# Kernel tuning notes

Hardware: AMD Instinct MI355X
Metric: run time of the kernel (lower is better)

## Reference

```python
import jax, jax.numpy as jnp
import numpy as np

B, S, D = 8, 1024, 768
H, HD = 12, 64  # heads, head dim (H*HD == D)
EPS = 1e-12


def setup_inputs() -> dict:
    key = jax.random.key(0)
    ks = jax.random.split(key, 8)
    s = 0.02
    return {
        "hidden_states": jax.random.normal(ks[0], (B, S, D), jnp.float32),
        "attention_mask": jnp.zeros((B, 1, 1, S), jnp.float32),
        "head_mask": jnp.ones((H,), jnp.float32),
        "Wq": jax.random.normal(ks[1], (D, H * HD), jnp.float32) * s,
        "bq": jnp.zeros((H * HD,), jnp.float32),
        "Wk": jax.random.normal(ks[2], (D, H * HD), jnp.float32) * s,
        "bk": jnp.zeros((H * HD,), jnp.float32),
        "Wv": jax.random.normal(ks[3], (D, H * HD), jnp.float32) * s,
        "bv": jnp.zeros((H * HD,), jnp.float32),
        "Wo": jax.random.normal(ks[4], (D, H * HD), jnp.float32) * s,  # torch Linear weight [out=D, in=H*HD]
        "bo": jnp.zeros((D,), jnp.float32),
        "gamma": jnp.ones((D,), jnp.float32),
        "beta": jnp.zeros((D,), jnp.float32),
    }


def reference(hidden_states, attention_mask, head_mask, Wq, bq, Wk, bk, Wv, bv, Wo, bo, gamma, beta):
    def heads(x):  # [B,S,H*HD] -> [B,H,S,HD]
        return x.reshape(B, S, H, HD).transpose(0, 2, 1, 3)

    q = heads(hidden_states @ Wq.T + bq)
    k = heads(hidden_states @ Wk.T + bk)
    v = heads(hidden_states @ Wv.T + bv)

    scores = jnp.einsum("bhqd,bhkd->bhqk", q, k) / np.sqrt(HD).astype(np.float32)
    scores = scores + attention_mask
    probs = jax.nn.softmax(scores, axis=-1)  # dropout p=0 (eval)
    ctx = jnp.einsum("bhqk,bhkd->bhqd", probs, v)  # [B,H,S,HD]

    # masked per-head output projection: Wo.T.view(H, HD, D)
    Wph = Wo.T.reshape(H, HD, D)
    proj = jnp.einsum("bhsd,hde,h->bse", ctx, Wph, head_mask) + bo

    # residual + LayerNorm
    x = proj + hidden_states
    mu = jnp.mean(x, axis=-1, keepdims=True)
    var = jnp.mean(jnp.square(x - mu), axis=-1, keepdims=True)
    out = (x - mu) * jax.lax.rsqrt(var + EPS) * gamma + beta
    return out
```

## Files before the change

kernel.cpp:

```cpp
#include <hip/hip_runtime.h>
#include <hip/hip_bf16.h>
#include <math.h>

#define Bn 8
#define Sn 1024
#define Dn 768
#define Hn 12
#define MROWS (Bn * Sn)

typedef __attribute__((ext_vector_type(8))) short short8;
typedef __attribute__((ext_vector_type(4))) float floatx4;

__device__ __forceinline__ unsigned short f2b(float x) {
    union { float f; unsigned u; } v; v.f = x;
    unsigned r = v.u + 0x7fffu + ((v.u >> 16) & 1u);
    return (unsigned short)(r >> 16);
}

__device__ __forceinline__ unsigned pk2(float a, float b) {
    union { __hip_bfloat162 h; unsigned u; } v;
    v.h = __float22bfloat162_rn(float2{a, b});
    return v.u;
}

__device__ __forceinline__ float fexp2(float x) {
    float r;
    asm("v_exp_f32 %0, %1" : "=v"(r) : "v"(x));
    return r;
}

__device__ __forceinline__ void gload16(const void* g, void* l) {
    __builtin_amdgcn_global_load_lds(
        (const __attribute__((address_space(1))) void*)g,
        (__attribute__((address_space(3))) void*)l, 16, 0, 0);
}

#define MEMFENCE() asm volatile("" ::: "memory")
#define WAITV8()  asm volatile("s_waitcnt vmcnt(8)" ::: "memory")
#define WAITV6()  asm volatile("s_waitcnt vmcnt(6)" ::: "memory")
#define WAITV0()  asm volatile("s_waitcnt vmcnt(0)" ::: "memory")
#define WAITLGKM() asm volatile("s_waitcnt lgkmcnt(0)" ::: "memory")

__global__ __launch_bounds__(256) void convert_all(const float* __restrict__ X,
                                                   const float* __restrict__ Wq, const float* __restrict__ Wk,
                                                   const float* __restrict__ Wv, const float* __restrict__ Wo,
                                                   unsigned short* __restrict__ Xb,
                                                   unsigned short* __restrict__ Wqb, unsigned short* __restrict__ Wkb,
                                                   unsigned short* __restrict__ Wvb, unsigned short* __restrict__ Wob) {
    const int id = blockIdx.x;
    const float* src;
    unsigned short* dst;
    int i;
    if (id < 6144) {
        src = X; dst = Xb;
        i = id * 256 + threadIdx.x;
    } else {
        const int y = (id - 6144) / 576;
        src = (y == 0) ? Wq : (y == 1) ? Wk : (y == 2) ? Wv : Wo;
        dst = (y == 0) ? Wqb : (y == 1) ? Wkb : (y == 2) ? Wvb : Wob;
        i = ((id - 6144) % 576) * 256 + threadIdx.x;
    }
    float4 v = reinterpret_cast<const float4*>(src)[i];
    ushort4 o;
    o.x = f2b(v.x); o.y = f2b(v.y); o.z = f2b(v.z); o.w = f2b(v.w);
    reinterpret_cast<ushort4*>(dst)[i] = o;
}

#define QKV_COMPUTE(Ab, Wb)                                                    \
    {                                                                          \
        short8 af[4][2], bf[4][2];                                             \
        _Pragma("unroll") for (int i = 0; i < 4; i++)                          \
            _Pragma("unroll") for (int ks = 0; ks < 2; ks++) {                 \
                af[i][ks] = *(const short8*)&(Ab)[aoff[i][ks]];                \
                bf[i][ks] = *(const short8*)&(Wb)[woff[i][ks]];                \
            }                                                                  \
        __builtin_amdgcn_s_setprio(1);                                         \
        _Pragma("unroll") for (int ks = 0; ks < 2; ks++)                       \
            _Pragma("unroll") for (int i = 0; i < 4; i++)                      \
                _Pragma("unroll") for (int j = 0; j < 4; j++)                  \
                    acc[i][j] = __builtin_amdgcn_mfma_f32_16x16x32_bf16(       \
                        af[i][ks], bf[j][ks], acc[i][j], 0, 0, 0);             \
        __builtin_amdgcn_s_setprio(0);                                         \
    }

__global__ __launch_bounds__(256) void gemm_qkv(const unsigned short* __restrict__ A,
                                                const unsigned short* __restrict__ Wq,
                                                const unsigned short* __restrict__ Wk,
                                                const unsigned short* __restrict__ Wv,
                                                const float* __restrict__ bq,
                                                const float* __restrict__ bk,
                                                const float* __restrict__ bv,
                                                unsigned short* __restrict__ Qh,
                                                unsigned short* __restrict__ Kh,
                                                unsigned short* __restrict__ Vt) {
    __shared__ __align__(16) unsigned short As[2][128 * 64];
    __shared__ __align__(16) unsigned short Ws[2][128 * 64];
    const int orig = blockIdx.x;
    const int chunk = orig & 7;
    const int local = orig >> 3;
    const int by = chunk * 8 + local / 18;
    const int bxr = local % 18;
    const int mat = bxr / 6;
    const int m0 = by * 128;
    const int n0 = (bxr % 6) * 128;
    const unsigned short* W = (mat == 0) ? Wq : (mat == 1) ? Wk : Wv;
    const float* bias = (mat == 0) ? bq : (mat == 1) ? bk : bv;
    unsigned short* Cout = (mat == 0) ? Qh : (mat == 1) ? Kh : Vt;

    const int tid = threadIdx.x;
    const int w = tid >> 6, l = tid & 63, quad = l >> 4, mr = l & 15;
    const int wm = (w >> 1) * 64, wn = (w & 1) * 64;

    const unsigned short* gAsrc[4];
    const unsigned short* gWsrc[4];
    unsigned short* lAdst[4];
    unsigned short* lWdst[4];
#pragma unroll
    for (int j = 0; j < 4; j++) {
        const int u = tid + j * 256;
        const int r = u >> 3, c = u & 7;
        const int kq = (c ^ (r & 7)) * 8;
        gAsrc[j] = &A[(size_t)(m0 + r) * Dn + kq];
        gWsrc[j] = &W[(size_t)(n0 + r) * Dn + kq];
        lAdst[j] = &As[0][u * 8];
        lWdst[j] = &Ws[0][u * 8];
    }

    int aoff[4][2], woff[4][2];
#pragma unroll
    for (int i = 0; i < 4; i++) {
        const int ra = wm + i * 16 + mr;
        const int rw = wn + i * 16 + mr;
#pragma unroll
        for (int ks = 0; ks < 2; ks++) {
            aoff[i][ks] = (ra * 8 + ((quad + ks * 4) ^ (ra & 7))) * 8;
            woff[i][ks] = (rw * 8 + ((quad + ks * 4) ^ (rw & 7))) * 8;
        }
    }

    floatx4 acc[4][4];
#pragma unroll
    for (int i = 0; i < 4; i++)
#pragma unroll
        for (int j = 0; j < 4; j++) {
            floatx4 z = {0.f, 0.f, 0.f, 0.f};
            acc[i][j] = z;
        }

    const unsigned short* Af = &As[0][0];
    const unsigned short* Wf = &Ws[0][0];

#pragma unroll
    for (int j = 0; j < 4; j++) {
        gload16(gAsrc[j], lAdst[j]);
        gload16(gWsrc[j], lWdst[j]);
    }

    for (int kt = 0; kt < 12; kt += 2) {
        {
            const int k0 = (kt + 1) * 64;
#pragma unroll
            for (int j = 0; j < 4; j++) {
                gload16(gAsrc[j] + k0, lAdst[j] + 8192);
                gload16(gWsrc[j] + k0, lWdst[j] + 8192);
            }
        }
        WAITV8();
        __builtin_amdgcn_s_barrier();
        MEMFENCE();
        QKV_COMPUTE(Af, Wf);
        __builtin_amdgcn_s_barrier();
        MEMFENCE();

        if (kt + 2 < 12) {
            const int k0 = (kt + 2) * 64;
#pragma unroll
            for (int j = 0; j < 4; j++) {
                gload16(gAsrc[j] + k0, lAdst[j]);
                gload16(gWsrc[j] + k0, lWdst[j]);
            }
            WAITV8();
        } else {
            WAITV0();
        }
        __builtin_amdgcn_s_barrier();
        MEMFENCE();
        QKV_COMPUTE(Af + 8192, Wf + 8192);
        __builtin_amdgcn_s_barrier();
        MEMFENCE();
    }

#pragma unroll
    for (int j = 0; j < 4; j++) {
        const int col = n0 + wn + j * 16 + mr;
        const float bval = bias[col];
        const int h = col >> 6, d = col & 63;
#pragma unroll
        for (int i = 0; i < 4; i++) {
            const int mbase = m0 + wm + i * 16 + quad * 4;
            const int b = mbase >> 10, s0 = mbase & 1023;
            const size_t base = (size_t)(b * Hn + h) << 16;
            if (mat == 2) {
                ushort4 o;
                o.x = f2b(acc[i][j][0] + bval);
                o.y = f2b(acc[i][j][1] + bval);
                o.z = f2b(acc[i][j][2] + bval);
                o.w = f2b(acc[i][j][3] + bval);
                *reinterpret_cast<ushort4*>(&Cout[base + (size_t)d * 1024 + s0]) = o;
            } else {
#pragma unroll
                for (int r = 0; r < 4; r++) {
                    const float val = acc[i][j][r] + bval;
                    Cout[base + (size_t)(s0 + r) * 64 + d] = f2b(val);
                }
            }
        }
    }
}

#define OUT_COMPUTE(Ab, Wb)                                                    \
    {                                                                          \
        short8 af[4][2], bf[2][2];                                             \
        _Pragma("unroll") for (int i = 0; i < 4; i++)                          \
            _Pragma("unroll") for (int ks = 0; ks < 2; ks++)                   \
                af[i][ks] = *(const short8*)&(Ab)[aoff[i][ks]];                \
        _Pragma("unroll") for (int j = 0; j < 2; j++)                          \
            _Pragma("unroll") for (int ks = 0; ks < 2; ks++)                   \
                bf[j][ks] = *(const short8*)&(Wb)[woff[j][ks]];                \
        __builtin_amdgcn_s_setprio(1);                                         \
        _Pragma("unroll") for (int ks = 0; ks < 2; ks++)                       \
            _Pragma("unroll") for (int i = 0; i < 4; i++)                      \
                _Pragma("unroll") for (int j = 0; j < 2; j++)                  \
                    acc[i][j] = __builtin_amdgcn_mfma_f32_16x16x32_bf16(       \
                        af[i][ks], bf[j][ks], acc[i][j], 0, 0, 0);             \
        __builtin_amdgcn_s_setprio(0);                                         \
    }

__global__ __launch_bounds__(256) void gemm_out(const unsigned short* __restrict__ A,
                                                const unsigned short* __restrict__ W,
                                                const float* __restrict__ bias,
                                                const float* __restrict__ X,
                                                float* __restrict__ xres) {
    __shared__ __align__(16) unsigned short As[2][64 * 64];
    __shared__ __align__(16) unsigned short Ws[2][128 * 64];
    const int orig = blockIdx.x;
    const int chunk = orig & 7;
    const int local = orig >> 3;
    const int by = chunk * 16 + local / 6;
    const int bx = local % 6;
    const int m0 = by * 64;
    const int n0 = bx * 128;

    const int tid = threadIdx.x;
    const int w = tid >> 6, l = tid & 63, quad = l >> 4, mr = l & 15;

    const unsigned short* gAsrc[2];
    unsigned short* lAdst[2];
#pragma unroll
    for (int j = 0; j < 2; j++) {
        const int u = tid + j * 256;
        const int r = u >> 3, c = u & 7;
        gAsrc[j] = &A[(size_t)(m0 + r) * Dn + (c ^ (r & 7)) * 8];
        lAdst[j] = &As[0][u * 8];
    }
    const unsigned short* gWsrc[4];
    unsigned short* lWdst[4];
#pragma unroll
    for (int j = 0; j < 4; j++) {
        const int u = tid + j * 256;
        const int r = u >> 3, c = u & 7;
        gWsrc[j] = &W[(size_t)(n0 + r) * Dn + (c ^ (r & 7)) * 8];
        lWdst[j] = &Ws[0][u * 8];
    }

    int aoff[4][2], woff[2][2];
#pragma unroll
    for (int i = 0; i < 4; i++) {
        const int ra = i * 16 + mr;
#pragma unroll
        for (int ks = 0; ks < 2; ks++)
            aoff[i][ks] = (ra * 8 + ((quad + ks * 4) ^ (ra & 7))) * 8;
    }
#pragma unroll
    for (int j = 0; j < 2; j++) {
        const int rw = w * 32 + j * 16 + mr;
#pragma unroll
        for (int ks = 0; ks < 2; ks++)
            woff[j][ks] = (rw * 8 + ((quad + ks * 4) ^ (rw & 7))) * 8;
    }

    floatx4 acc[4][2];
#pragma unroll
    for (int i = 0; i < 4; i++)
#pragma unroll
        for (int j = 0; j < 2; j++) {
            floatx4 z = {0.f, 0.f, 0.f, 0.f};
            acc[i][j] = z;
        }

    const unsigned short* Af = &As[0][0];
    const unsigned short* Wf = &Ws[0][0];

#pragma unroll
    for (int j = 0; j < 2; j++) gload16(gAsrc[j], lAdst[j]);
#pragma unroll
    for (int j = 0; j < 4; j++) gload16(gWsrc[j], lWdst[j]);

    for (int kt = 0; kt < 12; kt += 2) {
        {
            const int k0 = (kt + 1) * 64;
#pragma unroll
            for (int j = 0; j < 2; j++) gload16(gAsrc[j] + k0, lAdst[j] + 4096);
#pragma unroll
            for (int j = 0; j < 4; j++) gload16(gWsrc[j] + k0, lWdst[j] + 8192);
        }
        WAITV6();
        __builtin_amdgcn_s_barrier();
        MEMFENCE();
        OUT_COMPUTE(Af, Wf);
        __builtin_amdgcn_s_barrier();
        MEMFENCE();

        if (kt + 2 < 12) {
            const int k0 = (kt + 2) * 64;
#pragma unroll
            for (int j = 0; j < 2; j++) gload16(gAsrc[j] + k0, lAdst[j]);
#pragma unroll
            for (int j = 0; j < 4; j++) gload16(gWsrc[j] + k0, lWdst[j]);
            WAITV6();
        } else {
            WAITV0();
        }
        __builtin_amdgcn_s_barrier();
        MEMFENCE();
        OUT_COMPUTE(Af + 4096, Wf + 8192);
        __builtin_amdgcn_s_barrier();
        MEMFENCE();
    }

#pragma unroll
    for (int j = 0; j < 2; j++) {
        const int col = n0 + w * 32 + j * 16 + mr;
        const float bval = bias[col];
#pragma unroll
        for (int i = 0; i < 4; i++) {
#pragma unroll
            for (int r = 0; r < 4; r++) {
                const int m = m0 + i * 16 + quad * 4 + r;
                xres[(size_t)m * Dn + col] = acc[i][j][r] + bval + X[(size_t)m * Dn + col];
            }
        }
    }
}

__global__ __launch_bounds__(256) void flash_attn_mfma(const unsigned short* __restrict__ Qh,
                                                       const unsigned short* __restrict__ Kh,
                                                       const unsigned short* __restrict__ Vt,
                                                       const float* __restrict__ mask,
                                                       const float* __restrict__ head_mask,
                                                       unsigned short* __restrict__ ctx) {
    __shared__ __align__(16) unsigned short Ks[64 * 72];
    __shared__ __align__(16) unsigned short Vs[64 * 72];
    __shared__ __align__(16) unsigned short Ps[128 * 72];
    __shared__ float msk[64];

    const float LOG2E = 1.44269504088896f;
    const float C1 = 0.125f * 1.44269504088896f;

    const int orig = blockIdx.x;
    const int chunk = orig & 7;
    const int local = orig >> 3;
    const int bh = chunk * 12 + local / 8;
    const int qt = local % 8;
    const int b = bh / Hn, h = bh % Hn;
    const int q0 = qt * 128;
    const int tid = threadIdx.x;
    const int w = tid >> 6, l = tid & 63, quad = l >> 4, mr = l & 15;
    const size_t hb = (size_t)(b * Hn + h) << 16;

    short8 aq[2][2];
#pragma unroll
    for (int j = 0; j < 2; j++)
#pragma unroll
        for (int ks = 0; ks < 2; ks++)
            aq[j][ks] = *(const short8*)&Qh[hb + (size_t)(q0 + w * 32 + j * 16 + mr) * 64 + ks * 32 + quad * 8];

    float l_s[2] = {0.f, 0.f};
    floatx4 oacc[2][4];
#pragma unroll
    for (int i = 0; i < 2; i++)
#pragma unroll
        for (int jj = 0; jj < 4; jj++) {
            floatx4 z = {0.f, 0.f, 0.f, 0.f};
            oacc[i][jj] = z;
        }

    const int srow = tid >> 2;
    const int scol = (tid & 3) * 16;

    short8 pk0 = *(const short8*)&Kh[hb + (size_t)srow * 64 + scol];
    short8 pk1 = *(const short8*)&Kh[hb + (size_t)srow * 64 + scol + 8];
    short8 pv0 = *(const short8*)&Vt[hb + (size_t)srow * 1024 + scol];
    short8 pv1 = *(const short8*)&Vt[hb + (size_t)srow * 1024 + scol + 8];
    float pm = mask[b * Sn + (tid & 63)];

    for (int kt = 0; kt < Sn / 64; kt++) {
        __builtin_amdgcn_s_barrier();
        MEMFENCE();
        *(short8*)&Ks[srow * 72 + scol] = pk0;
        *(short8*)&Ks[srow * 72 + scol + 8] = pk1;
        *(short8*)&Vs[srow * 72 + scol] = pv0;
        *(short8*)&Vs[srow * 72 + scol + 8] = pv1;
        if (tid < 64) msk[tid] = pm * LOG2E;
        if (kt < Sn / 64 - 1) {
            const int k0 = (kt + 1) * 64;
            pk0 = *(const short8*)&Kh[hb + (size_t)(k0 + srow) * 64 + scol];
            pk1 = *(const short8*)&Kh[hb + (size_t)(k0 + srow) * 64 + scol + 8];
            pv0 = *(const short8*)&Vt[hb + (size_t)srow * 1024 + k0 + scol];
            pv1 = *(const short8*)&Vt[hb + (size_t)srow * 1024 + k0 + scol + 8];
            pm = mask[b * Sn + k0 + (tid & 63)];
        }
        WAITLGKM();
        __builtin_amdgcn_s_barrier();
        MEMFENCE();

        floatx4 sacc[4][2];
#pragma unroll
        for (int i = 0; i < 4; i++)
#pragma unroll
            for (int j = 0; j < 2; j++) {
                floatx4 z = {0.f, 0.f, 0.f, 0.f};
                sacc[i][j] = z;
            }
#pragma unroll
        for (int ks = 0; ks < 2; ks++) {
            short8 kfr[4];
#pragma unroll
            for (int i = 0; i < 4; i++)
                kfr[i] = *(const short8*)&Ks[(i * 16 + mr) * 72 + ks * 32 + quad * 8];
            __builtin_amdgcn_s_setprio(1);
#pragma unroll
            for (int i = 0; i < 4; i++)
#pragma unroll
                for (int j = 0; j < 2; j++)
                    sacc[i][j] = __builtin_amdgcn_mfma_f32_16x16x32_bf16(kfr[i], aq[j][ks], sacc[i][j], 0, 0, 0);
            __builtin_amdgcn_s_setprio(0);
        }

#pragma unroll
        for (int i = 0; i < 4; i++) {
            floatx4 mk4 = *(const floatx4*)&msk[i * 16 + quad * 4];
#pragma unroll
            for (int j = 0; j < 2; j++) {
                float p[4];
#pragma unroll
                for (int r = 0; r < 4; r++) {
                    p[r] = fexp2(sacc[i][j][r] * C1 + mk4[r]);
                    l_s[j] += p[r];
                }
                uint2 w2;
                w2.x = pk2(p[0], p[1]);
                w2.y = pk2(p[2], p[3]);
                *(uint2*)&Ps[(w * 32 + j * 16 + mr) * 72 + i * 16 + quad * 4] = w2;
            }
        }

#pragma unroll
        for (int ks = 0; ks < 2; ks++) {
            short8 ap0 = *(const short8*)&Ps[(w * 32 + mr) * 72 + ks * 32 + quad * 8];
            short8 ap1 = *(const short8*)&Ps[(w * 32 + 16 + mr) * 72 + ks * 32 + quad * 8];
            __builtin_amdgcn_s_setprio(1);
#pragma unroll
            for (int jj = 0; jj < 4; jj++) {
                short8 bv = *(const short8*)&Vs[(jj * 16 + mr) * 72 + ks * 32 + quad * 8];
                oacc[0][jj] = __builtin_amdgcn_mfma_f32_16x16x32_bf16(ap0, bv, oacc[0][jj], 0, 0, 0);
                oacc[1][jj] = __builtin_amdgcn_mfma_f32_16x16x32_bf16(ap1, bv, oacc[1][jj], 0, 0, 0);
            }
            __builtin_amdgcn_s_setprio(0);
        }
    }

    float L[2];
#pragma unroll
    for (int j = 0; j < 2; j++) {
        float t = l_s[j];
        t += __shfl_xor(t, 16);
        t += __shfl_xor(t, 32);
        L[j] = t;
    }
    const float hm = head_mask[h];
    float inv[2][4];
#pragma unroll
    for (int i = 0; i < 2; i++)
#pragma unroll
        for (int r = 0; r < 4; r++)
            inv[i][r] = hm / __shfl(L[i], quad * 4 + r);

#pragma unroll
    for (int i = 0; i < 2; i++)
#pragma unroll
        for (int jj = 0; jj < 4; jj++)
#pragma unroll
            for (int r = 0; r < 4; r++) {
                const int qrow = q0 + w * 32 + i * 16 + quad * 4 + r;
                ctx[(size_t)(b * Sn + qrow) * Dn + h * 64 + jj * 16 + mr] = f2b(oacc[i][jj][r] * inv[i][r]);
            }
}

__global__ __launch_bounds__(256) void ln_kernel(const float* __restrict__ x,
                                                 const float* __restrict__ gamma,
                                                 const float* __restrict__ beta,
                                                 float* __restrict__ out) {
    __shared__ float r1[4];
    __shared__ float r2[4];
    const int m = blockIdx.x;
    const int tid = threadIdx.x;
    const int w = tid >> 6, lane = tid & 63;

    float xv[3];
    float s = 0.f, ss = 0.f;
#pragma unroll
    for (int i = 0; i < 3; i++) {
        int j = tid + i * 256;
        float t = x[(size_t)m * Dn + j];
        xv[i] = t;
        s += t;
        ss += t * t;
    }
#pragma unroll
    for (int o = 1; o < 64; o <<= 1) {
        s += __shfl_xor(s, o);
        ss += __shfl_xor(ss, o);
    }
    if (lane == 0) { r1[w] = s; r2[w] = ss; }
    __syncthreads();
    const float sum = r1[0] + r1[1] + r1[2] + r1[3];
    const float sqs = r2[0] + r2[1] + r2[2] + r2[3];
    const float mu = sum * (1.0f / Dn);
    const float var = sqs * (1.0f / Dn) - mu * mu;
    const float rstd = rsqrtf(var + 1e-12f);
#pragma unroll
    for (int i = 0; i < 3; i++) {
        int j = tid + i * 256;
        out[(size_t)m * Dn + j] = (xv[i] - mu) * rstd * gamma[j] + beta[j];
    }
}

extern "C" void kernel_launch(void* const* d_in, const int* in_sizes, int n_in,
                              void* d_out, int out_size, void* d_ws, size_t ws_size,
                              hipStream_t stream) {
    const float* X         = (const float*)d_in[0];
    const float* mask      = (const float*)d_in[1];
    const float* head_mask = (const float*)d_in[2];
    const float* Wq        = (const float*)d_in[3];
    const float* bq        = (const float*)d_in[4];
    const float* Wk        = (const float*)d_in[5];
    const float* bk        = (const float*)d_in[6];
    const float* Wv        = (const float*)d_in[7];
    const float* bv        = (const float*)d_in[8];
    const float* Wo        = (const float*)d_in[9];
    const float* bo        = (const float*)d_in[10];
    const float* gamma     = (const float*)d_in[11];
    const float* beta      = (const float*)d_in[12];
    float* out = (float*)d_out;

    const size_t NE = (size_t)Bn * Sn * Dn;
    const size_t NW = (size_t)Dn * Dn;

    char* p = (char*)d_ws;
    unsigned short* Xb  = (unsigned short*)p;  p += NE * 2;
    unsigned short* Wqb = (unsigned short*)p;  p += NW * 2;
    unsigned short* Wkb = (unsigned short*)p;  p += NW * 2;
    unsigned short* Wvb = (unsigned short*)p;  p += NW * 2;
    unsigned short* Wob = (unsigned short*)p;  p += NW * 2;
    unsigned short* Qh  = (unsigned short*)p;  p += NE * 2;
    unsigned short* Kh  = (unsigned short*)p;  p += NE * 2;
    unsigned short* Vtb = (unsigned short*)p;  p += NE * 2;
    unsigned short* ctx = (unsigned short*)p;  p += NE * 2;
    float* xres = (float*)p;

    convert_all<<<8448, 256, 0, stream>>>(X, Wq, Wk, Wv, Wo, Xb, Wqb, Wkb, Wvb, Wob);

    gemm_qkv<<<1152, 256, 0, stream>>>(Xb, Wqb, Wkb, Wvb, bq, bk, bv, Qh, Kh, Vtb);

    flash_attn_mfma<<<768, 256, 0, stream>>>(Qh, Kh, Vtb, mask, head_mask, ctx);

    gemm_out<<<768, 256, 0, stream>>>(ctx, Wob, bo, X, xres);

    ln_kernel<<<MROWS, 256, 0, stream>>>(xres, gamma, beta, out);
}
```

Measured before the change: 215.3 us.

## Enlarge GEMM tiles to 256x256 and 128x256 with 512-thread blocks

Both projection GEMMs now use 512-thread blocks with larger output tiles. The QKV GEMM goes from 128x128 to 256x256 with 8x4 MFMA tiles per wave, and the output GEMM goes from 64x128 to 128x256 with 4x4 tiles per wave. The inner MFMA loop is reordered to load one B fragment at a time, which eases register pressure. The aim is more data reuse per LDS load and fewer global loads per FLOP. The cost is far fewer blocks (288 and 192 on a device with about 256 CUs), which risks poor occupancy and wave-quantization imbalance, plus much higher LDS and register use.

```diff
diff --git a/kernel.cpp b/kernel.cpp
--- a/kernel.cpp
+++ b/kernel.cpp
@@ -68,48 +68,49 @@
 
 #define QKV_COMPUTE(Ab, Wb)                                                    \
     {                                                                          \
-        short8 af[4][2], bf[4][2];                                             \
-        _Pragma("unroll") for (int i = 0; i < 4; i++)                          \
-            _Pragma("unroll") for (int ks = 0; ks < 2; ks++) {                 \
-                af[i][ks] = *(const short8*)&(Ab)[aoff[i][ks]];                \
-                bf[i][ks] = *(const short8*)&(Wb)[woff[i][ks]];                \
+        _Pragma("unroll") for (int ks = 0; ks < 2; ks++) {                     \
+            short8 af[8];                                                      \
+            _Pragma("unroll") for (int i = 0; i < 8; i++)                      \
+                af[i] = *(const short8*)&(Ab)[aoff[i][ks]];                    \
+            __builtin_amdgcn_s_setprio(1);                                     \
+            _Pragma("unroll") for (int j = 0; j < 4; j++) {                    \
+                short8 bf = *(const short8*)&(Wb)[woff[j][ks]];                \
+                _Pragma("unroll") for (int i = 0; i < 8; i++)                  \
+                    acc[i][j] = __builtin_amdgcn_mfma_f32_16x16x32_bf16(       \
+                        af[i], bf, acc[i][j], 0, 0, 0);                        \
             }                                                                  \
-        __builtin_amdgcn_s_setprio(1);                                         \
-        _Pragma("unroll") for (int ks = 0; ks < 2; ks++)                       \
-            _Pragma("unroll") for (int i = 0; i < 4; i++)                      \
-                _Pragma("unroll") for (int j = 0; j < 4; j++)                  \
-                    acc[i][j] = __builtin_amdgcn_mfma_f32_16x16x32_bf16(       \
-                        af[i][ks], bf[j][ks], acc[i][j], 0, 0, 0);             \
-        __builtin_amdgcn_s_setprio(0);                                         \
-    }
-
-__global__ __launch_bounds__(256) void gemm_qkv(const unsigned short* __restrict__ A,
-                                                const unsigned short* __restrict__ Wq,
-                                                const unsigned short* __restrict__ Wk,
-                                                const unsigned short* __restrict__ Wv,
-                                                const float* __restrict__ bq,
-                                                const float* __restrict__ bk,
-                                                const float* __restrict__ bv,
-                                                unsigned short* __restrict__ Qh,
-                                                unsigned short* __restrict__ Kh,
-                                                unsigned short* __restrict__ Vt) {
-    __shared__ __align__(16) unsigned short As[2][128 * 64];
-    __shared__ __align__(16) unsigned short Ws[2][128 * 64];
+            __builtin_amdgcn_s_setprio(0);                                     \
+        }                                                                      \
+    }
+
+__global__ __launch_bounds__(512, 2) void gemm_qkv(const unsigned short* __restrict__ A,
+                                                   const unsigned short* __restrict__ Wq,
+                                                   const unsigned short* __restrict__ Wk,
+                                                   const unsigned short* __restrict__ Wv,
+                                                   const float* __restrict__ bq,
+                                                   const float* __restrict__ bk,
+                                                   const float* __restrict__ bv,
+                                                   unsigned short* __restrict__ Qh,
+                                                   unsigned short* __restrict__ Kh,
+                                                   unsigned short* __restrict__ Vt) {
+    __shared__ __align__(16) unsigned short As[2][256 * 64];
+    __shared__ __align__(16) unsigned short Ws[2][256 * 64];
     const int orig = blockIdx.x;
     const int chunk = orig & 7;
     const int local = orig >> 3;
-    const int by = chunk * 8 + local / 18;
-    const int bxr = local % 18;
-    const int mat = bxr / 6;
-    const int m0 = by * 128;
-    const int n0 = (bxr % 6) * 128;
+    const int by = chunk * 4 + local / 9;
+    const int bxr = local % 9;
+    const int mat = bxr / 3;
+    const int m0 = by * 256;
+    const int n0 = (bxr % 3) * 256;
     const unsigned short* W = (mat == 0) ? Wq : (mat == 1) ? Wk : Wv;
     const float* bias = (mat == 0) ? bq : (mat == 1) ? bk : bv;
     unsigned short* Cout = (mat == 0) ? Qh : (mat == 1) ? Kh : Vt;
 
     const int tid = threadIdx.x;
     const int w = tid >> 6, l = tid & 63, quad = l >> 4, mr = l & 15;
-    const int wm = (w >> 1) * 64, wn = (w & 1) * 64;
+    const int wm = (w >> 2) * 128;
+    const int wn = (w & 3) * 64;
 
     const unsigned short* gAsrc[4];
     const unsigned short* gWsrc[4];
@@ -117,7 +118,7 @@
     unsigned short* lWdst[4];
 #pragma unroll
     for (int j = 0; j < 4; j++) {
-        const int u = tid + j * 256;
+        const int u = tid + j * 512;
         const int r = u >> 3, c = u & 7;
         const int kq = (c ^ (r & 7)) * 8;
         gAsrc[j] = &A[(size_t)(m0 + r) * Dn + kq];
@@ -126,21 +127,25 @@
         lWdst[j] = &Ws[0][u * 8];
     }
 
-    int aoff[4][2], woff[4][2];
-#pragma unroll
-    for (int i = 0; i < 4; i++) {
+    int aoff[8][2], woff[4][2];
+#pragma unroll
+    for (int i = 0; i < 8; i++) {
         const int ra = wm + i * 16 + mr;
-        const int rw = wn + i * 16 + mr;
-#pragma unroll
-        for (int ks = 0; ks < 2; ks++) {
+#pragma unroll
+        for (int ks = 0; ks < 2; ks++)
             aoff[i][ks] = (ra * 8 + ((quad + ks * 4) ^ (ra & 7))) * 8;
-            woff[i][ks] = (rw * 8 + ((quad + ks * 4) ^ (rw & 7))) * 8;
-        }
-    }
-
-    floatx4 acc[4][4];
-#pragma unroll
-    for (int i = 0; i < 4; i++)
+    }
+#pragma unroll
+    for (int j = 0; j < 4; j++) {
+        const int rw = wn + j * 16 + mr;
+#pragma unroll
+        for (int ks = 0; ks < 2; ks++)
+            woff[j][ks] = (rw * 8 + ((quad + ks * 4) ^ (rw & 7))) * 8;
+    }
+
+    floatx4 acc[8][4];
+#pragma unroll
+    for (int i = 0; i < 8; i++)
 #pragma unroll
         for (int j = 0; j < 4; j++) {
             floatx4 z = {0.f, 0.f, 0.f, 0.f};
@@ -161,8 +166,8 @@
             const int k0 = (kt + 1) * 64;
 #pragma unroll
             for (int j = 0; j < 4; j++) {
-                gload16(gAsrc[j] + k0, lAdst[j] + 8192);
-                gload16(gWsrc[j] + k0, lWdst[j] + 8192);
+                gload16(gAsrc[j] + k0, lAdst[j] + 16384);
+                gload16(gWsrc[j] + k0, lWdst[j] + 16384);
             }
         }
         WAITV8();
@@ -185,7 +190,7 @@
         }
         __builtin_amdgcn_s_barrier();
         MEMFENCE();
-        QKV_COMPUTE(Af + 8192, Wf + 8192);
+        QKV_COMPUTE(Af + 16384, Wf + 16384);
         __builtin_amdgcn_s_barrier();
         MEMFENCE();
     }
@@ -196,7 +201,7 @@
         const float bval = bias[col];
         const int h = col >> 6, d = col & 63;
 #pragma unroll
-        for (int i = 0; i < 4; i++) {
+        for (int i = 0; i < 8; i++) {
             const int mbase = m0 + wm + i * 16 + quad * 4;
             const int b = mbase >> 10, s0 = mbase & 1023;
             const size_t base = (size_t)(b * Hn + h) << 16;
@@ -220,45 +225,46 @@
 
 #define OUT_COMPUTE(Ab, Wb)                                                    \
     {                                                                          \
-        short8 af[4][2], bf[2][2];                                             \
-        _Pragma("unroll") for (int i = 0; i < 4; i++)                          \
-            _Pragma("unroll") for (int ks = 0; ks < 2; ks++)                   \
-                af[i][ks] = *(const short8*)&(Ab)[aoff[i][ks]];                \
-        _Pragma("unroll") for (int j = 0; j < 2; j++)                          \
-            _Pragma("unroll") for (int ks = 0; ks < 2; ks++)                   \
-                bf[j][ks] = *(const short8*)&(Wb)[woff[j][ks]];                \
-        __builtin_amdgcn_s_setprio(1);                                         \
-        _Pragma("unroll") for (int ks = 0; ks < 2; ks++)                       \
+        _Pragma("unroll") for (int ks = 0; ks < 2; ks++) {                     \
+            short8 af[4];                                                      \
             _Pragma("unroll") for (int i = 0; i < 4; i++)                      \
-                _Pragma("unroll") for (int j = 0; j < 2; j++)                  \
+                af[i] = *(const short8*)&(Ab)[aoff[i][ks]];                    \
+            __builtin_amdgcn_s_setprio(1);                                     \
+            _Pragma("unroll") for (int j = 0; j < 4; j++) {                    \
+                short8 bf = *(const short8*)&(Wb)[woff[j][ks]];                \
+                _Pragma("unroll") for (int i = 0; i < 4; i++)                  \
                     acc[i][j] = __builtin_amdgcn_mfma_f32_16x16x32_bf16(       \
-                        af[i][ks], bf[j][ks], acc[i][j], 0, 0, 0);             \
-        __builtin_amdgcn_s_setprio(0);                                         \
-    }
-
-__global__ __launch_bounds__(256) void gemm_out(const unsigned short* __restrict__ A,
-                                                const unsigned short* __restrict__ W,
-                                                const float* __restrict__ bias,
-                                                const float* __restrict__ X,
-                                                float* __restrict__ xres) {
-    __shared__ __align__(16) unsigned short As[2][64 * 64];
-    __shared__ __align__(16) unsigned short Ws[2][128 * 64];
+                        af[i], bf, acc[i][j], 0, 0, 0);                        \
+            }                                                                  \
+            __builtin_amdgcn_s_setprio(0);                                     \
+        }                                                                      \
+    }
+
+__global__ __launch_bounds__(512, 2) void gemm_out(const unsigned short* __restrict__ A,
+                                                   const unsigned short* __restrict__ W,
+                                                   const float* __restrict__ bias,
+                                                   const float* __restrict__ X,
+                                                   float* __restrict__ xres) {
+    __shared__ __align__(16) unsigned short As[2][128 * 64];
+    __shared__ __align__(16) unsigned short Ws[2][256 * 64];
     const int orig = blockIdx.x;
     const int chunk = orig & 7;
     const int local = orig >> 3;
-    const int by = chunk * 16 + local / 6;
-    const int bx = local % 6;
-    const int m0 = by * 64;
-    const int n0 = bx * 128;
+    const int by = chunk * 8 + local / 3;
+    const int bx = local % 3;
+    const int m0 = by * 128;
+    const int n0 = bx * 256;
 
     const int tid = threadIdx.x;
     const int w = tid >> 6, l = tid & 63, quad = l >> 4, mr = l & 15;
+    const int wm = (w >> 2) * 64;
+    const int wn = (w & 3) * 64;
 
     const unsigned short* gAsrc[2];
     unsigned short* lAdst[2];
 #pragma unroll
     for (int j = 0; j < 2; j++) {
-        const int u = tid + j * 256;
+        const int u = tid + j * 512;
         const int r = u >> 3, c = u & 7;
         gAsrc[j] = &A[(size_t)(m0 + r) * Dn + (c ^ (r & 7)) * 8];
         lAdst[j] = &As[0][u * 8];
@@ -267,33 +273,33 @@
     unsigned short* lWdst[4];
 #pragma unroll
     for (int j = 0; j < 4; j++) {
-        const int u = tid + j * 256;
+        const int u = tid + j * 512;
         const int r = u >> 3, c = u & 7;
         gWsrc[j] = &W[(size_t)(n0 + r) * Dn + (c ^ (r & 7)) * 8];
         lWdst[j] = &Ws[0][u * 8];
     }
 
-    int aoff[4][2], woff[2][2];
+    int aoff[4][2], woff[4][2];
 #pragma unroll
     for (int i = 0; i < 4; i++) {
-        const int ra = i * 16 + mr;
+        const int ra = wm + i * 16 + mr;
 #pragma unroll
         for (int ks = 0; ks < 2; ks++)
             aoff[i][ks] = (ra * 8 + ((quad + ks * 4) ^ (ra & 7))) * 8;
     }
 #pragma unroll
-    for (int j = 0; j < 2; j++) {
-        const int rw = w * 32 + j * 16 + mr;
+    for (int j = 0; j < 4; j++) {
+        const int rw = wn + j * 16 + mr;
 #pragma unroll
         for (int ks = 0; ks < 2; ks++)
             woff[j][ks] = (rw * 8 + ((quad + ks * 4) ^ (rw & 7))) * 8;
     }
 
-    floatx4 acc[4][2];
+    floatx4 acc[4][4];
 #pragma unroll
     for (int i = 0; i < 4; i++)
 #pragma unroll
-        for (int j = 0; j < 2; j++) {
+        for (int j = 0; j < 4; j++) {
             floatx4 z = {0.f, 0.f, 0.f, 0.f};
             acc[i][j] = z;
         }
@@ -310,9 +316,9 @@
         {
             const int k0 = (kt + 1) * 64;
 #pragma unroll
-            for (int j = 0; j < 2; j++) gload16(gAsrc[j] + k0, lAdst[j] + 4096);
-#pragma unroll
-            for (int j = 0; j < 4; j++) gload16(gWsrc[j] + k0, lWdst[j] + 8192);
+            for (int j = 0; j < 2; j++) gload16(gAsrc[j] + k0, lAdst[j] + 8192);
+#pragma unroll
+            for (int j = 0; j < 4; j++) gload16(gWsrc[j] + k0, lWdst[j] + 16384);
         }
         WAITV6();
         __builtin_amdgcn_s_barrier();
@@ -333,20 +339,20 @@
         }
         __builtin_amdgcn_s_barrier();
         MEMFENCE();
-        OUT_COMPUTE(Af + 4096, Wf + 8192);
-        __builtin_amdgcn_s_barrier();
-        MEMFENCE();
-    }
-
-#pragma unroll
-    for (int j = 0; j < 2; j++) {
-        const int col = n0 + w * 32 + j * 16 + mr;
+        OUT_COMPUTE(Af + 8192, Wf + 16384);
+        __builtin_amdgcn_s_barrier();
+        MEMFENCE();
+    }
+
+#pragma unroll
+    for (int j = 0; j < 4; j++) {
+        const int col = n0 + wn + j * 16 + mr;
         const float bval = bias[col];
 #pragma unroll
         for (int i = 0; i < 4; i++) {
 #pragma unroll
             for (int r = 0; r < 4; r++) {
-                const int m = m0 + i * 16 + quad * 4 + r;
+                const int m = m0 + wm + i * 16 + quad * 4 + r;
                 xres[(size_t)m * Dn + col] = acc[i][j][r] + bval + X[(size_t)m * Dn + col];
             }
         }
@@ -581,11 +587,11 @@
 
     convert_all<<<8448, 256, 0, stream>>>(X, Wq, Wk, Wv, Wo, Xb, Wqb, Wkb, Wvb, Wob);
 
-    gemm_qkv<<<1152, 256, 0, stream>>>(Xb, Wqb, Wkb, Wvb, bq, bk, bv, Qh, Kh, Vtb);
+    gemm_qkv<<<288, 512, 0, stream>>>(Xb, Wqb, Wkb, Wvb, bq, bk, bv, Qh, Kh, Vtb);
 
     flash_attn_mfma<<<768, 256, 0, stream>>>(Qh, Kh, Vtb, mask, head_mask, ctx);
 
-    gemm_out<<<768, 256, 0, stream>>>(ctx, Wob, bo, X, xres);
+    gemm_out<<<192, 512, 0, stream>>>(ctx, Wob, bo, X, xres);
 
     ln_kernel<<<MROWS, 256, 0, stream>>>(xres, gamma, beta, out);
 }
```

Result: slower. 268.2 us (+24.6%).

## Retile QKV and output GEMMs with K=32 stages and larger block tiles

Applied to the files above, without the earlier changes.

The QKV GEMM moves to 512-thread blocks covering 256x128 output tiles with a K step of 32, which halves the grid. The output GEMM moves from 64x128 to 128x128 tiles with a 2x2 warp layout, also with a K step of 32. LDS tiles shrink to 32-wide rows with a new XOR swizzle, and the wait counts are adjusted to match. The aim is more reuse of each loaded tile per block and less LDS per stage, so more blocks can be resident. The cost is twice as many barrier-synchronised K iterations and fewer MFMAs between syncs.

```diff
diff --git a/kernel.cpp b/kernel.cpp
--- a/kernel.cpp
+++ b/kernel.cpp
@@ -36,10 +36,11 @@
 }
 
 #define MEMFENCE() asm volatile("" ::: "memory")
-#define WAITV8()  asm volatile("s_waitcnt vmcnt(8)" ::: "memory")
-#define WAITV6()  asm volatile("s_waitcnt vmcnt(6)" ::: "memory")
+#define WAITV3()  asm volatile("s_waitcnt vmcnt(3)" ::: "memory")
+#define WAITV4()  asm volatile("s_waitcnt vmcnt(4)" ::: "memory")
 #define WAITV0()  asm volatile("s_waitcnt vmcnt(0)" ::: "memory")
 #define WAITLGKM() asm volatile("s_waitcnt lgkmcnt(0)" ::: "memory")
+
 
 __global__ __launch_bounds__(256) void convert_all(const float* __restrict__ X,
                                                    const float* __restrict__ Wq, const float* __restrict__ Wk,
@@ -68,40 +69,38 @@
 
 #define QKV_COMPUTE(Ab, Wb)                                                    \
     {                                                                          \
-        short8 af[4][2], bf[4][2];                                             \
-        _Pragma("unroll") for (int i = 0; i < 4; i++)                          \
-            _Pragma("unroll") for (int ks = 0; ks < 2; ks++) {                 \
-                af[i][ks] = *(const short8*)&(Ab)[aoff[i][ks]];                \
-                bf[i][ks] = *(const short8*)&(Wb)[woff[i][ks]];                \
-            }                                                                  \
+        short8 bf[4];                                                          \
+        _Pragma("unroll") for (int j = 0; j < 4; j++)                          \
+            bf[j] = *(const short8*)&(Wb)[woff[j]];                            \
         __builtin_amdgcn_s_setprio(1);                                         \
-        _Pragma("unroll") for (int ks = 0; ks < 2; ks++)                       \
-            _Pragma("unroll") for (int i = 0; i < 4; i++)                      \
-                _Pragma("unroll") for (int j = 0; j < 4; j++)                  \
-                    acc[i][j] = __builtin_amdgcn_mfma_f32_16x16x32_bf16(       \
-                        af[i][ks], bf[j][ks], acc[i][j], 0, 0, 0);             \
+        _Pragma("unroll") for (int i = 0; i < 4; i++) {                        \
+            short8 af = *(const short8*)&(Ab)[aoff[i]];                        \
+            _Pragma("unroll") for (int j = 0; j < 4; j++)                      \
+                acc[i][j] = __builtin_amdgcn_mfma_f32_16x16x32_bf16(           \
+                    af, bf[j], acc[i][j], 0, 0, 0);                            \
+        }                                                                      \
         __builtin_amdgcn_s_setprio(0);                                         \
     }
 
-__global__ __launch_bounds__(256) void gemm_qkv(const unsigned short* __restrict__ A,
-                                                const unsigned short* __restrict__ Wq,
-                                                const unsigned short* __restrict__ Wk,
-                                                const unsigned short* __restrict__ Wv,
-                                                const float* __restrict__ bq,
-                                                const float* __restrict__ bk,
-                                                const float* __restrict__ bv,
-                                                unsigned short* __restrict__ Qh,
-                                                unsigned short* __restrict__ Kh,
-                                                unsigned short* __restrict__ Vt) {
-    __shared__ __align__(16) unsigned short As[2][128 * 64];
-    __shared__ __align__(16) unsigned short Ws[2][128 * 64];
+__global__ __launch_bounds__(512, 4) void gemm_qkv(const unsigned short* __restrict__ A,
+                                                   const unsigned short* __restrict__ Wq,
+                                                   const unsigned short* __restrict__ Wk,
+                                                   const unsigned short* __restrict__ Wv,
+                                                   const float* __restrict__ bq,
+                                                   const float* __restrict__ bk,
+                                                   const float* __restrict__ bv,
+                                                   unsigned short* __restrict__ Qh,
+                                                   unsigned short* __restrict__ Kh,
+                                                   unsigned short* __restrict__ Vt) {
+    __shared__ __align__(16) unsigned short As[2][256 * 32];
+    __shared__ __align__(16) unsigned short Ws[2][128 * 32];
     const int orig = blockIdx.x;
     const int chunk = orig & 7;
     const int local = orig >> 3;
-    const int by = chunk * 8 + local / 18;
+    const int by = chunk * 4 + local / 18;
     const int bxr = local % 18;
     const int mat = bxr / 6;
-    const int m0 = by * 128;
+    const int m0 = by * 256;
     const int n0 = (bxr % 6) * 128;
     const unsigned short* W = (mat == 0) ? Wq : (mat == 1) ? Wk : Wv;
     const float* bias = (mat == 0) ? bq : (mat == 1) ? bk : bv;
@@ -109,33 +108,39 @@
 
     const int tid = threadIdx.x;
     const int w = tid >> 6, l = tid & 63, quad = l >> 4, mr = l & 15;
-    const int wm = (w >> 1) * 64, wn = (w & 1) * 64;
-
-    const unsigned short* gAsrc[4];
-    const unsigned short* gWsrc[4];
-    unsigned short* lAdst[4];
-    unsigned short* lWdst[4];
-#pragma unroll
-    for (int j = 0; j < 4; j++) {
-        const int u = tid + j * 256;
-        const int r = u >> 3, c = u & 7;
-        const int kq = (c ^ (r & 7)) * 8;
-        gAsrc[j] = &A[(size_t)(m0 + r) * Dn + kq];
-        gWsrc[j] = &W[(size_t)(n0 + r) * Dn + kq];
+    const int wm = (w >> 1) * 64;
+    const int wn = (w & 1) * 64;
+
+    const unsigned short* gAsrc[2];
+    unsigned short* lAdst[2];
+#pragma unroll
+    for (int j = 0; j < 2; j++) {
+        const int u = tid + j * 512;
+        const int r = u >> 2, c = u & 3;
+        const int cp = c ^ ((r >> 1) & 3);
+        gAsrc[j] = &A[(size_t)(m0 + r) * Dn + cp * 8];
         lAdst[j] = &As[0][u * 8];
-        lWdst[j] = &Ws[0][u * 8];
-    }
-
-    int aoff[4][2], woff[4][2];
+    }
+    const unsigned short* gWsrc;
+    unsigned short* lWdst;
+    {
+        const int u = tid;
+        const int r = u >> 2, c = u & 3;
+        const int cp = c ^ ((r >> 1) & 3);
+        gWsrc = &W[(size_t)(n0 + r) * Dn + cp * 8];
+        lWdst = &Ws[0][u * 8];
+    }
+
+    int aoff[4], woff[4];
 #pragma unroll
     for (int i = 0; i < 4; i++) {
         const int ra = wm + i * 16 + mr;
-        const int rw = wn + i * 16 + mr;
-#pragma unroll
-        for (int ks = 0; ks < 2; ks++) {
-            aoff[i][ks] = (ra * 8 + ((quad + ks * 4) ^ (ra & 7))) * 8;
-            woff[i][ks] = (rw * 8 + ((quad + ks * 4) ^ (rw & 7))) * 8;
-        }
+        aoff[i] = (ra * 4 + (quad ^ ((ra >> 1) & 3))) * 8;
+    }
+#pragma unroll
+    for (int j = 0; j < 4; j++) {
+        const int rw = wn + j * 16 + mr;
+        woff[j] = (rw * 4 + (quad ^ ((rw >> 1) & 3))) * 8;
     }
 
     floatx4 acc[4][4];
@@ -150,42 +155,36 @@
     const unsigned short* Af = &As[0][0];
     const unsigned short* Wf = &Ws[0][0];
 
-#pragma unroll
-    for (int j = 0; j < 4; j++) {
-        gload16(gAsrc[j], lAdst[j]);
-        gload16(gWsrc[j], lWdst[j]);
-    }
-
-    for (int kt = 0; kt < 12; kt += 2) {
+    gload16(gAsrc[0], lAdst[0]);
+    gload16(gAsrc[1], lAdst[1]);
+    gload16(gWsrc, lWdst);
+
+    for (int kt = 0; kt < 24; kt += 2) {
         {
-            const int k0 = (kt + 1) * 64;
-#pragma unroll
-            for (int j = 0; j < 4; j++) {
-                gload16(gAsrc[j] + k0, lAdst[j] + 8192);
-                gload16(gWsrc[j] + k0, lWdst[j] + 8192);
-            }
-        }
-        WAITV8();
+            const int k0 = (kt + 1) * 32;
+            gload16(gAsrc[0] + k0, lAdst[0] + 8192);
+            gload16(gAsrc[1] + k0, lAdst[1] + 8192);
+            gload16(gWsrc + k0, lWdst + 4096);
+        }
+        WAITV3();
         __builtin_amdgcn_s_barrier();
         MEMFENCE();
         QKV_COMPUTE(Af, Wf);
         __builtin_amdgcn_s_barrier();
         MEMFENCE();
 
-        if (kt + 2 < 12) {
-            const int k0 = (kt + 2) * 64;
-#pragma unroll
-            for (int j = 0; j < 4; j++) {
-                gload16(gAsrc[j] + k0, lAdst[j]);
-                gload16(gWsrc[j] + k0, lWdst[j]);
-            }
-            WAITV8();
+        if (kt + 2 < 24) {
+            const int k0 = (kt + 2) * 32;
+            gload16(gAsrc[0] + k0, lAdst[0]);
+            gload16(gAsrc[1] + k0, lAdst[1]);
+            gload16(gWsrc + k0, lWdst);
+            WAITV3();
         } else {
             WAITV0();
         }
         __builtin_amdgcn_s_barrier();
         MEMFENCE();
-        QKV_COMPUTE(Af + 8192, Wf + 8192);
+        QKV_COMPUTE(Af + 8192, Wf + 4096);
         __builtin_amdgcn_s_barrier();
         MEMFENCE();
     }
@@ -220,80 +219,71 @@
 
 #define OUT_COMPUTE(Ab, Wb)                                                    \
     {                                                                          \
-        short8 af[4][2], bf[2][2];                                             \
-        _Pragma("unroll") for (int i = 0; i < 4; i++)                          \
-            _Pragma("unroll") for (int ks = 0; ks < 2; ks++)                   \
-                af[i][ks] = *(const short8*)&(Ab)[aoff[i][ks]];                \
-        _Pragma("unroll") for (int j = 0; j < 2; j++)                          \
-            _Pragma("unroll") for (int ks = 0; ks < 2; ks++)                   \
-                bf[j][ks] = *(const short8*)&(Wb)[woff[j][ks]];                \
+        short8 bf[4];                                                          \
+        _Pragma("unroll") for (int j = 0; j < 4; j++)                          \
+            bf[j] = *(const short8*)&(Wb)[woff[j]];                            \
         __builtin_amdgcn_s_setprio(1);                                         \
-        _Pragma("unroll") for (int ks = 0; ks < 2; ks++)                       \
-            _Pragma("unroll") for (int i = 0; i < 4; i++)                      \
-                _Pragma("unroll") for (int j = 0; j < 2; j++)                  \
-                    acc[i][j] = __builtin_amdgcn_mfma_f32_16x16x32_bf16(       \
-                        af[i][ks], bf[j][ks], acc[i][j], 0, 0, 0);             \
+        _Pragma("unroll") for (int i = 0; i < 4; i++) {                        \
+            short8 af = *(const short8*)&(Ab)[aoff[i]];                        \
+            _Pragma("unroll") for (int j = 0; j < 4; j++)                      \
+                acc[i][j] = __builtin_amdgcn_mfma_f32_16x16x32_bf16(           \
+                    af, bf[j], acc[i][j], 0, 0, 0);                            \
+        }                                                                      \
         __builtin_amdgcn_s_setprio(0);                                         \
     }
 
-__global__ __launch_bounds__(256) void gemm_out(const unsigned short* __restrict__ A,
-                                                const unsigned short* __restrict__ W,
-                                                const float* __restrict__ bias,
-                                                const float* __restrict__ X,
-                                                float* __restrict__ xres) {
-    __shared__ __align__(16) unsigned short As[2][64 * 64];
-    __shared__ __align__(16) unsigned short Ws[2][128 * 64];
+__global__ __launch_bounds__(256, 4) void gemm_out(const unsigned short* __restrict__ A,
+                                                   const unsigned short* __restrict__ W,
+                                                   const float* __restrict__ bias,
+                                                   const float* __restrict__ X,
+                                                   float* __restrict__ xres) {
+    __shared__ __align__(16) unsigned short As[2][128 * 32];
+    __shared__ __align__(16) unsigned short Ws[2][128 * 32];
     const int orig = blockIdx.x;
     const int chunk = orig & 7;
     const int local = orig >> 3;
-    const int by = chunk * 16 + local / 6;
+    const int by = chunk * 8 + local / 6;
     const int bx = local % 6;
-    const int m0 = by * 64;
+    const int m0 = by * 128;
     const int n0 = bx * 128;
 
     const int tid = threadIdx.x;
     const int w = tid >> 6, l = tid & 63, quad = l >> 4, mr = l & 15;
+    const int wm = (w >> 1) * 64;
+    const int wn = (w & 1) * 64;
 
     const unsigned short* gAsrc[2];
     unsigned short* lAdst[2];
+    const unsigned short* gWsrc[2];
+    unsigned short* lWdst[2];
 #pragma unroll
     for (int j = 0; j < 2; j++) {
         const int u = tid + j * 256;
-        const int r = u >> 3, c = u & 7;
-        gAsrc[j] = &A[(size_t)(m0 + r) * Dn + (c ^ (r & 7)) * 8];
+        const int r = u >> 2, c = u & 3;
+        const int cp = c ^ ((r >> 1) & 3);
+        gAsrc[j] = &A[(size_t)(m0 + r) * Dn + cp * 8];
         lAdst[j] = &As[0][u * 8];
-    }
-    const unsigned short* gWsrc[4];
-    unsigned short* lWdst[4];
+        gWsrc[j] = &W[(size_t)(n0 + r) * Dn + cp * 8];
+        lWdst[j] = &Ws[0][u * 8];
+    }
+
+    int aoff[4], woff[4];
+#pragma unroll
+    for (int i = 0; i < 4; i++) {
+        const int ra = wm + i * 16 + mr;
+        aoff[i] = (ra * 4 + (quad ^ ((ra >> 1) & 3))) * 8;
+    }
 #pragma unroll
     for (int j = 0; j < 4; j++) {
-        const int u = tid + j * 256;
-        const int r = u >> 3, c = u & 7;
-        gWsrc[j] = &W[(size_t)(n0 + r) * Dn + (c ^ (r & 7)) * 8];
-        lWdst[j] = &Ws[0][u * 8];
-    }
-
-    int aoff[4][2], woff[2][2];
-#pragma unroll
-    for (int i = 0; i < 4; i++) {
-        const int ra = i * 16 + mr;
-#pragma unroll
-        for (int ks = 0; ks < 2; ks++)
-            aoff[i][ks] = (ra * 8 + ((quad + ks * 4) ^ (ra & 7))) * 8;
-    }
-#pragma unroll
-    for (int j = 0; j < 2; j++) {
-        const int rw = w * 32 + j * 16 + mr;
-#pragma unroll
-        for (int ks = 0; ks < 2; ks++)
-            woff[j][ks] = (rw * 8 + ((quad + ks * 4) ^ (rw & 7))) * 8;
-    }
-
-    floatx4 acc[4][2];
+        const int rw = wn + j * 16 + mr;
+        woff[j] = (rw * 4 + (quad ^ ((rw >> 1) & 3))) * 8;
+    }
+
+    floatx4 acc[4][4];
 #pragma unroll
     for (int i = 0; i < 4; i++)
 #pragma unroll
-        for (int j = 0; j < 2; j++) {
+        for (int j = 0; j < 4; j++) {
             floatx4 z = {0.f, 0.f, 0.f, 0.f};
             acc[i][j] = z;
         }
@@ -302,51 +292,51 @@
     const unsigned short* Wf = &Ws[0][0];
 
 #pragma unroll
-    for (int j = 0; j < 2; j++) gload16(gAsrc[j], lAdst[j]);
-#pragma unroll
-    for (int j = 0; j < 4; j++) gload16(gWsrc[j], lWdst[j]);
-
-    for (int kt = 0; kt < 12; kt += 2) {
+    for (int j = 0; j < 2; j++) { gload16(gAsrc[j], lAdst[j]); gload16(gWsrc[j], lWdst[j]); }
+
+    for (int kt = 0; kt < 24; kt += 2) {
         {
-            const int k0 = (kt + 1) * 64;
-#pragma unroll
-            for (int j = 0; j < 2; j++) gload16(gAsrc[j] + k0, lAdst[j] + 4096);
-#pragma unroll
-            for (int j = 0; j < 4; j++) gload16(gWsrc[j] + k0, lWdst[j] + 8192);
-        }
-        WAITV6();
+            const int k0 = (kt + 1) * 32;
+#pragma unroll
+            for (int j = 0; j < 2; j++) {
+                gload16(gAsrc[j] + k0, lAdst[j] + 4096);
+                gload16(gWsrc[j] + k0, lWdst[j] + 4096);
+            }
+        }
+        WAITV4();
         __builtin_amdgcn_s_barrier();
         MEMFENCE();
         OUT_COMPUTE(Af, Wf);
         __builtin_amdgcn_s_barrier();
         MEMFENCE();
 
-        if (kt + 2 < 12) {
-            const int k0 = (kt + 2) * 64;
-#pragma unroll
-            for (int j = 0; j < 2; j++) gload16(gAsrc[j] + k0, lAdst[j]);
-#pragma unroll
-            for (int j = 0; j < 4; j++) gload16(gWsrc[j] + k0, lWdst[j]);
-            WAITV6();
+        if (kt + 2 < 24) {
+            const int k0 = (kt + 2) * 32;
+#pragma unroll
+            for (int j = 0; j < 2; j++) {
+                gload16(gAsrc[j] + k0, lAdst[j]);
+                gload16(gWsrc[j] + k0, lWdst[j]);
+            }
+            WAITV4();
         } else {
             WAITV0();
         }
         __builtin_amdgcn_s_barrier();
         MEMFENCE();
-        OUT_COMPUTE(Af + 4096, Wf + 8192);
-        __builtin_amdgcn_s_barrier();
-        MEMFENCE();
-    }
-
-#pragma unroll
-    for (int j = 0; j < 2; j++) {
-        const int col = n0 + w * 32 + j * 16 + mr;
+        OUT_COMPUTE(Af + 4096, Wf + 4096);
+        __builtin_amdgcn_s_barrier();
+        MEMFENCE();
+    }
+
+#pragma unroll
+    for (int j = 0; j < 4; j++) {
+        const int col = n0 + wn + j * 16 + mr;
         const float bval = bias[col];
 #pragma unroll
         for (int i = 0; i < 4; i++) {
 #pragma unroll
             for (int r = 0; r < 4; r++) {
-                const int m = m0 + i * 16 + quad * 4 + r;
+                const int m = m0 + wm + i * 16 + quad * 4 + r;
                 xres[(size_t)m * Dn + col] = acc[i][j][r] + bval + X[(size_t)m * Dn + col];
             }
         }
@@ -581,11 +571,11 @@
 
     convert_all<<<8448, 256, 0, stream>>>(X, Wq, Wk, Wv, Wo, Xb, Wqb, Wkb, Wvb, Wob);
 
-    gemm_qkv<<<1152, 256, 0, stream>>>(Xb, Wqb, Wkb, Wvb, bq, bk, bv, Qh, Kh, Vtb);
+    gemm_qkv<<<576, 512, 0, stream>>>(Xb, Wqb, Wkb, Wvb, bq, bk, bv, Qh, Kh, Vtb);
 
     flash_attn_mfma<<<768, 256, 0, stream>>>(Qh, Kh, Vtb, mask, head_mask, ctx);
 
-    gemm_out<<<768, 256, 0, stream>>>(ctx, Wob, bo, X, xres);
+    gemm_out<<<384, 256, 0, stream>>>(ctx, Wob, bo, X, xres);
 
     ln_kernel<<<MROWS, 256, 0, stream>>>(xres, gamma, beta, out);
 }
```

After: 226.3 us. 5.1% more time.
